# Performance work log

Hardware: AMD Instinct MI355X
Metric: run time of the kernel (lower is better)

## Reference

```python
import jax, jax.numpy as jnp
import numpy as np

B, T, D = 32, 512, 64   # batch, timesteps, latent dim
H, S = 64, 4096         # hidden_size, state_dim
EPS = 1e-6              # flax LayerNorm default epsilon


def _glorot(k, shape):
    lim = np.sqrt(6.0 / (shape[0] + shape[1])).astype(np.float32)
    return jax.random.uniform(k, shape, jnp.float32, -lim, lim)


def setup_inputs() -> dict:
    key = jax.random.key(0)
    ks = jax.random.split(key, 7)
    # gate order in the fused 4H axis: i, f, g, o ; flax inits f-gate bias to 1
    bh = jnp.concatenate([jnp.zeros((H,)), jnp.ones((H,)), jnp.zeros((2 * H,))]).astype(jnp.float32)
    return {
        "enc_outputs": jax.random.normal(ks[0], (B, T, D), jnp.float32),
        "Wx": _glorot(ks[1], (D, 4 * H)),   # input->gates, no bias (flax dense_i)
        "Wh": _glorot(ks[2], (H, 4 * H)),   # hidden->gates
        "bh": bh,
        "W1": _glorot(ks[3], (H, 2 * H)), "b1": jnp.zeros((2 * H,), jnp.float32),
        "g1": jnp.ones((2 * H,), jnp.float32), "be1": jnp.zeros((2 * H,), jnp.float32),
        "W2": _glorot(ks[4], (2 * H, 2 * H)), "b2": jnp.zeros((2 * H,), jnp.float32),
        "g2": jnp.ones((2 * H,), jnp.float32), "be2": jnp.zeros((2 * H,), jnp.float32),
        "Wo": _glorot(ks[5], (2 * H, S)), "bo": jnp.zeros((S,), jnp.float32),
    }


def _layernorm(x, g, b):
    m = x.mean(-1, keepdims=True)
    v = ((x - m) ** 2).mean(-1, keepdims=True)
    return (x - m) * jax.lax.rsqrt(v + EPS) * g + b


def _lstm(enc, Wx, Wh, bh):
    # precompute all input projections in one big GEMM: [B,T,4H]
    xg = jnp.einsum('btd,dg->btg', enc, Wx)

    def step(carry, x_t):
        c, h = carry
        z = x_t + h @ Wh + bh              # [B,4H]
        i, f, g, o = jnp.split(z, 4, axis=-1)
        c = jax.nn.sigmoid(f) * c + jax.nn.sigmoid(i) * jnp.tanh(g)
        h = jax.nn.sigmoid(o) * jnp.tanh(c)
        return (c, h), h

    b = enc.shape[0]
    init = (jnp.zeros((b, H), enc.dtype), jnp.zeros((b, H), enc.dtype))
    _, hs = jax.lax.scan(step, init, xg.swapaxes(0, 1))  # hs: [T,B,H]
    return hs.swapaxes(0, 1)                              # [B,T,H]


def reference(enc_outputs, Wx, Wh, bh, W1, b1, g1, be1, W2, b2, g2, be2, Wo, bo):
    b, t, _ = enc_outputs.shape
    dec = _lstm(enc_outputs, Wx, Wh, bh)            # [B,T,H]
    flat = dec.reshape(b * t, H)
    h = jax.nn.gelu(_layernorm(flat @ W1 + b1, g1, be1))   # flax gelu: tanh approx
    # dropout deterministic (train=False) -> identity
    h = jax.nn.gelu(_layernorm(h @ W2 + b2, g2, be2))
    out = h @ Wo + bo                                # [B*T,S]
    return out.reshape(b, t, S)
```

## Files before the change

kernel.cpp:

```cpp
#include <hip/hip_runtime.h>
#include <hip/hip_bf16.h>

#define T_ 512

typedef __attribute__((ext_vector_type(8))) short short8;
typedef __attribute__((ext_vector_type(4))) float f32x4;

__device__ __forceinline__ float fast_rcp(float x){ return __builtin_amdgcn_rcpf(x); }
__device__ __forceinline__ float sigmoid_f(float x){
  return fast_rcp(1.f + __expf(-x));
}
__device__ __forceinline__ float tanh_f(float x){
  return fmaf(2.f, fast_rcp(1.f + __expf(-2.f*x)), -1.f);
}
__device__ __forceinline__ float gelu_f(float x){
  float u = 0.7978845608028654f*(x + 0.044715f*x*x*x);
  return 0.5f*x*(1.f + tanh_f(u));
}
__device__ __forceinline__ unsigned short bf16_bits(float x){
  __hip_bfloat16 b = __float2bfloat16(x);
  return __builtin_bit_cast(unsigned short, b);
}
__device__ __forceinline__ float bits_f32(unsigned short u){
  return __uint_as_float(((unsigned)u) << 16);
}
__device__ __forceinline__ void bar_lds(){
  asm volatile("s_waitcnt lgkmcnt(0)\n\ts_barrier" ::: "memory");
}

__global__ __launch_bounds__(256) void k_encT(const float* __restrict__ enc,
                                              unsigned short* __restrict__ encB)
{
  int i = blockIdx.x*256 + threadIdx.x;
  int b = i >> 15, t = (i >> 6) & 511, d = i & 63;
  float v = enc[i];
  unsigned short hi = bf16_bits(v);
  float rem = v - bits_f32(hi);
  unsigned short lo = bf16_bits(rem);
  size_t o = (size_t)t*4096 + b*128 + d;
  encB[o]      = hi;
  encB[o + 64] = lo;
}

__global__ __launch_bounds__(256) void k_whxT(const float* __restrict__ Wh,
                                              const float* __restrict__ Wx,
                                              unsigned short* __restrict__ WhxT)
{
  int i = blockIdx.x*256 + threadIdx.x;
  int j = i >> 7, k = i & 127;
  float v = (k < 64) ? Wh[k*256 + j] : Wx[(k - 64)*256 + j];
  WhxT[i] = bf16_bits(v);
}

__global__ __launch_bounds__(256, 1) void k_lstm(const unsigned short* __restrict__ encB,
                                                 const unsigned short* __restrict__ WhxT,
                                                 const float* __restrict__ bh,
                                                 unsigned short* __restrict__ hsb)
{
  __shared__ __align__(16) unsigned short Hb[2][16][72];
  int tid = threadIdx.x;
  int w = tid >> 6, l = tid & 63;
  int m = l & 15, q = l >> 4;
  int bo = blockIdx.x * 16;
  int col0 = 16*w + 4*q;

  const short* Wr = (const short*)WhxT;
  short8 ah[4][2], ax[4][2];
#pragma unroll
  for (int g = 0; g < 4; ++g)
#pragma unroll
    for (int kk = 0; kk < 2; ++kk){
      ah[g][kk] = *(const short8*)(Wr + (64*g + 16*w + m)*128 +      kk*32 + q*8);
      ax[g][kk] = *(const short8*)(Wr + (64*g + 16*w + m)*128 + 64 + kk*32 + q*8);
    }
  f32x4 bb[4];
#pragma unroll
  for (int g = 0; g < 4; ++g){
    bb[g][0] = bh[64*g + 16*w + 4*q + 0];
    bb[g][1] = bh[64*g + 16*w + 4*q + 1];
    bb[g][2] = bh[64*g + 16*w + 4*q + 2];
    bb[g][3] = bh[64*g + 16*w + 4*q + 3];
  }

  for (int i = tid; i < 576; i += 256) ((unsigned int*)&Hb[0][0][0])[i] = 0;

  const unsigned short* encp = encB;
  int em = (bo + m)*128;
  unsigned short* hsrow = hsb + ((size_t)(bo + m)*512)*64 + col0;

  short8 EA0,EA1,EA2,EA3, EB0,EB1,EB2,EB3, EC0,EC1,EC2,EC3, ED0,ED1,ED2,ED3;
  short8 e0,e1,e2,e3;
  e0 = *(const short8*)(encp + 0*4096 + em      + q*8);
  e1 = *(const short8*)(encp + 0*4096 + em + 32 + q*8);
  e2 = *(const short8*)(encp + 0*4096 + em + 64 + q*8);
  e3 = *(const short8*)(encp + 0*4096 + em + 96 + q*8);
  EB0 = *(const short8*)(encp + 1*4096 + em      + q*8);
  EB1 = *(const short8*)(encp + 1*4096 + em + 32 + q*8);
  EB2 = *(const short8*)(encp + 1*4096 + em + 64 + q*8);
  EB3 = *(const short8*)(encp + 1*4096 + em + 96 + q*8);
  EC0 = *(const short8*)(encp + 2*4096 + em      + q*8);
  EC1 = *(const short8*)(encp + 2*4096 + em + 32 + q*8);
  EC2 = *(const short8*)(encp + 2*4096 + em + 64 + q*8);
  EC3 = *(const short8*)(encp + 2*4096 + em + 96 + q*8);
  ED0 = *(const short8*)(encp + 3*4096 + em      + q*8);
  ED1 = *(const short8*)(encp + 3*4096 + em + 32 + q*8);
  ED2 = *(const short8*)(encp + 3*4096 + em + 64 + q*8);
  ED3 = *(const short8*)(encp + 3*4096 + em + 96 + q*8);

  f32x4 xacc[4];
#pragma unroll
  for (int g = 0; g < 4; ++g){
    f32x4 a = __builtin_amdgcn_mfma_f32_16x16x32_bf16(ax[g][0], e0, bb[g], 0,0,0);
    a = __builtin_amdgcn_mfma_f32_16x16x32_bf16(ax[g][1], e1, a, 0,0,0);
    a = __builtin_amdgcn_mfma_f32_16x16x32_bf16(ax[g][0], e2, a, 0,0,0);
    xacc[g] = __builtin_amdgcn_mfma_f32_16x16x32_bf16(ax[g][1], e3, a, 0,0,0);
  }
  float c0 = 0.f, c1 = 0.f, c2 = 0.f, c3 = 0.f;
  __syncthreads();

#define STEP(tt, EU0,EU1,EU2,EU3, EL0,EL1,EL2,EL3)                             \
  {                                                                            \
    const unsigned short* hb = &Hb[(tt) & 1][0][0];                            \
    short8 hv0 = *(const short8*)(hb + m*72 +      q*8);                       \
    short8 hv1 = *(const short8*)(hb + m*72 + 32 + q*8);                       \
    if ((tt) + 4 < T_){                                                        \
      const unsigned short* ep = encp + (size_t)((tt)+4)*4096 + em;            \
      EL0 = *(const short8*)(ep +      q*8);                                   \
      EL1 = *(const short8*)(ep + 32 + q*8);                                   \
      EL2 = *(const short8*)(ep + 64 + q*8);                                   \
      EL3 = *(const short8*)(ep + 96 + q*8);                                   \
    }                                                                          \
    f32x4 z0 = __builtin_amdgcn_mfma_f32_16x16x32_bf16(ah[0][0], hv0, xacc[0], 0,0,0); \
    f32x4 z1 = __builtin_amdgcn_mfma_f32_16x16x32_bf16(ah[1][0], hv0, xacc[1], 0,0,0); \
    f32x4 z2 = __builtin_amdgcn_mfma_f32_16x16x32_bf16(ah[2][0], hv0, xacc[2], 0,0,0); \
    f32x4 z3 = __builtin_amdgcn_mfma_f32_16x16x32_bf16(ah[3][0], hv0, xacc[3], 0,0,0); \
    z0 = __builtin_amdgcn_mfma_f32_16x16x32_bf16(ah[0][1], hv1, z0, 0,0,0);    \
    z1 = __builtin_amdgcn_mfma_f32_16x16x32_bf16(ah[1][1], hv1, z1, 0,0,0);    \
    z2 = __builtin_amdgcn_mfma_f32_16x16x32_bf16(ah[2][1], hv1, z2, 0,0,0);    \
    z3 = __builtin_amdgcn_mfma_f32_16x16x32_bf16(ah[3][1], hv1, z3, 0,0,0);    \
    float h0, h1, h2, h3;                                                      \
    { float si=sigmoid_f(z0[0]), sf=sigmoid_f(z1[0]);                          \
      float tg=tanh_f(z2[0]),    so=sigmoid_f(z3[0]);                          \
      c0 = sf*c0 + si*tg; h0 = so*tanh_f(c0); }                                \
    { float si=sigmoid_f(z0[1]), sf=sigmoid_f(z1[1]);                          \
      float tg=tanh_f(z2[1]),    so=sigmoid_f(z3[1]);                          \
      c1 = sf*c1 + si*tg; h1 = so*tanh_f(c1); }                                \
    { float si=sigmoid_f(z0[2]), sf=sigmoid_f(z1[2]);                          \
      float tg=tanh_f(z2[2]),    so=sigmoid_f(z3[2]);                          \
      c2 = sf*c2 + si*tg; h2 = so*tanh_f(c2); }                                \
    { float si=sigmoid_f(z0[3]), sf=sigmoid_f(z1[3]);                          \
      float tg=tanh_f(z2[3]),    so=sigmoid_f(z3[3]);                          \
      c3 = sf*c3 + si*tg; h3 = so*tanh_f(c3); }                                \
    ushort4 hp;                                                                \
    hp.x = bf16_bits(h0); hp.y = bf16_bits(h1);                                \
    hp.z = bf16_bits(h2); hp.w = bf16_bits(h3);                                \
    *(ushort4*)(&Hb[((tt)+1) & 1][m][col0]) = hp;                              \
    *(ushort4*)(hsrow + (size_t)(tt)*64) = hp;                                 \
    xacc[0] = __builtin_amdgcn_mfma_f32_16x16x32_bf16(ax[0][0], EU0, bb[0], 0,0,0); \
    xacc[1] = __builtin_amdgcn_mfma_f32_16x16x32_bf16(ax[1][0], EU0, bb[1], 0,0,0); \
    xacc[2] = __builtin_amdgcn_mfma_f32_16x16x32_bf16(ax[2][0], EU0, bb[2], 0,0,0); \
    xacc[3] = __builtin_amdgcn_mfma_f32_16x16x32_bf16(ax[3][0], EU0, bb[3], 0,0,0); \
    xacc[0] = __builtin_amdgcn_mfma_f32_16x16x32_bf16(ax[0][1], EU1, xacc[0], 0,0,0); \
    xacc[1] = __builtin_amdgcn_mfma_f32_16x16x32_bf16(ax[1][1], EU1, xacc[1], 0,0,0); \
    xacc[2] = __builtin_amdgcn_mfma_f32_16x16x32_bf16(ax[2][1], EU1, xacc[2], 0,0,0); \
    xacc[3] = __builtin_amdgcn_mfma_f32_16x16x32_bf16(ax[3][1], EU1, xacc[3], 0,0,0); \
    xacc[0] = __builtin_amdgcn_mfma_f32_16x16x32_bf16(ax[0][0], EU2, xacc[0], 0,0,0); \
    xacc[1] = __builtin_amdgcn_mfma_f32_16x16x32_bf16(ax[1][0], EU2, xacc[1], 0,0,0); \
    xacc[2] = __builtin_amdgcn_mfma_f32_16x16x32_bf16(ax[2][0], EU2, xacc[2], 0,0,0); \
    xacc[3] = __builtin_amdgcn_mfma_f32_16x16x32_bf16(ax[3][0], EU2, xacc[3], 0,0,0); \
    xacc[0] = __builtin_amdgcn_mfma_f32_16x16x32_bf16(ax[0][1], EU3, xacc[0], 0,0,0); \
    xacc[1] = __builtin_amdgcn_mfma_f32_16x16x32_bf16(ax[1][1], EU3, xacc[1], 0,0,0); \
    xacc[2] = __builtin_amdgcn_mfma_f32_16x16x32_bf16(ax[2][1], EU3, xacc[2], 0,0,0); \
    xacc[3] = __builtin_amdgcn_mfma_f32_16x16x32_bf16(ax[3][1], EU3, xacc[3], 0,0,0); \
    bar_lds();                          \
  }

  for (int t = 0; t < T_; t += 4){
    STEP(t,   EB0,EB1,EB2,EB3, EA0,EA1,EA2,EA3);
    STEP(t+1, EC0,EC1,EC2,EC3, EB0,EB1,EB2,EB3);
    STEP(t+2, ED0,ED1,ED2,ED3, EC0,EC1,EC2,EC3);
    STEP(t+3, EA0,EA1,EA2,EA3, ED0,ED1,ED2,ED3);
  }
#undef STEP
}

__global__ __launch_bounds__(256) void k_mlp(const unsigned short* __restrict__ hsb,
    const float* __restrict__ W1, const float* __restrict__ b1,
    const float* __restrict__ g1, const float* __restrict__ be1,
    const float* __restrict__ W2, const float* __restrict__ b2,
    const float* __restrict__ g2, const float* __restrict__ be2,
    __hip_bfloat16* __restrict__ h2g)
{
  __shared__ __align__(16) float xs[2][64];
  __shared__ __align__(16) float vs[2][128];
  __shared__ float red[2][2][2];
  int tid = threadIdx.x;
  int jj = tid & 127, rg = tid >> 7;
  int lane = tid & 63;
  int whalf = (tid >> 6) & 1;
  float w1c[64], w2c[128];
#pragma unroll
  for (int k = 0; k < 64; ++k) w1c[k] = W1[k*128 + jj];
#pragma unroll
  for (int k = 0; k < 128; ++k) w2c[k] = W2[k*128 + jj];
  float b1j = b1[jj], g1j = g1[jj], be1j = be1[jj];
  float b2j = b2[jj], g2j = g2[jj], be2j = be2[jj];
  int base = blockIdx.x * 64;
  for (int p = 0; p < 32; ++p){
    int r = base + p*2 + rg;
    if (whalf == 0) xs[rg][lane] = bits_f32(hsb[(size_t)r*64 + lane]);
    __syncthreads();
    float a0 = b1j, a1 = 0.f;
    const float4* x4 = (const float4*)xs[rg];
#pragma unroll
    for (int k4 = 0; k4 < 16; ++k4){
      float4 v = x4[k4];
      a0 = fmaf(v.x, w1c[4*k4+0], a0);
      a1 = fmaf(v.y, w1c[4*k4+1], a1);
      a0 = fmaf(v.z, w1c[4*k4+2], a0);
      a1 = fmaf(v.w, w1c[4*k4+3], a1);
    }
    float a = a0 + a1;
    float s1 = a, s2 = a*a;
#pragma unroll
    for (int off = 32; off > 0; off >>= 1){
      s1 += __shfl_xor(s1, off, 64);
      s2 += __shfl_xor(s2, off, 64);
    }
    if (lane == 0){ red[rg][whalf][0] = s1; red[rg][whalf][1] = s2; }
    __syncthreads();
    s1 = red[rg][0][0] + red[rg][1][0];
    s2 = red[rg][0][1] + red[rg][1][1];
    float mean = s1*(1.f/128.f);
    float var  = s2*(1.f/128.f) - mean*mean;
    float rstd = rsqrtf(var + 1e-6f);
    float y = gelu_f((a - mean)*rstd*g1j + be1j);
    vs[rg][jj] = y;
    __syncthreads();
    float c0 = b2j, c1 = 0.f;
    const float4* v4 = (const float4*)vs[rg];
#pragma unroll
    for (int k4 = 0; k4 < 32; ++k4){
      float4 v = v4[k4];
      c0 = fmaf(v.x, w2c[4*k4+0], c0);
      c1 = fmaf(v.y, w2c[4*k4+1], c1);
      c0 = fmaf(v.z, w2c[4*k4+2], c0);
      c1 = fmaf(v.w, w2c[4*k4+3], c1);
    }
    float cc = c0 + c1;
    float t1 = cc, t2 = cc*cc;
#pragma unroll
    for (int off = 32; off > 0; off >>= 1){
      t1 += __shfl_xor(t1, off, 64);
      t2 += __shfl_xor(t2, off, 64);
    }
    if (lane == 0){ red[rg][whalf][0] = t1; red[rg][whalf][1] = t2; }
    __syncthreads();
    t1 = red[rg][0][0] + red[rg][1][0];
    t2 = red[rg][0][1] + red[rg][1][1];
    mean = t1*(1.f/128.f);
    var  = t2*(1.f/128.f) - mean*mean;
    rstd = rsqrtf(var + 1e-6f);
    float z = gelu_f((cc - mean)*rstd*g2j + be2j);
    h2g[(size_t)r*128 + jj] = __float2bfloat16(z);
  }
}

__global__ __launch_bounds__(256) void k_wot(const float* __restrict__ Wo,
                                             __hip_bfloat16* __restrict__ WoT)
{
  __shared__ __hip_bfloat16 tl[64][130];
  int tid = threadIdx.x;
  int n0 = blockIdx.x * 64;
  for (int idx = tid; idx < 64*128; idx += 256){
    int k = idx >> 6, nl = idx & 63;
    tl[nl][k] = __float2bfloat16(Wo[(size_t)k*4096 + n0 + nl]);
  }
  __syncthreads();
  for (int idx = tid; idx < 64*128; idx += 256){
    int nl = idx >> 7, k = idx & 127;
    WoT[(size_t)(n0 + nl)*128 + k] = tl[nl][k];
  }
}

__global__ __launch_bounds__(256) void k_out(const __hip_bfloat16* __restrict__ h2g,
                                             const __hip_bfloat16* __restrict__ WoT,
                                             const float* __restrict__ bo,
                                             float* __restrict__ out)
{
  int bid0 = blockIdx.x;
  int bid = (bid0 & 7)*512 + (bid0 >> 3);
  int Mb = bid >> 5, Nb = bid & 31;
  int tid = threadIdx.x;
  int w = tid >> 6, l = tid & 63;
  int wm = w >> 1, wn = w & 1;
  int m0 = Mb*128 + wm*64, n0 = Nb*128 + wn*64;
  int lr = l & 15, lk = (l >> 4)*8;
  f32x4 acc[4][4] = {};
  const short* A  = (const short*)WoT;
  const short* Bp = (const short*)h2g;
#pragma unroll
  for (int kk = 0; kk < 4; ++kk){
    int ko = kk*32 + lk;
    short8 av[4], bv[4];
#pragma unroll
    for (int i = 0; i < 4; ++i) av[i] = *(const short8*)(A  + (size_t)(n0 + i*16 + lr)*128 + ko);
#pragma unroll
    for (int i = 0; i < 4; ++i) bv[i] = *(const short8*)(Bp + (size_t)(m0 + i*16 + lr)*128 + ko);
#pragma unroll
    for (int fm = 0; fm < 4; ++fm)
#pragma unroll
      for (int fn = 0; fn < 4; ++fn)
        acc[fm][fn] = __builtin_amdgcn_mfma_f32_16x16x32_bf16(av[fn], bv[fm], acc[fm][fn], 0, 0, 0);
  }
  int nb_ = (l >> 4)*4;
#pragma unroll
  for (int fn = 0; fn < 4; ++fn){
    f32x4 bia = *(const f32x4*)(bo + n0 + fn*16 + nb_);
#pragma unroll
    for (int fm = 0; fm < 4; ++fm){
      size_t row = (size_t)(m0 + fm*16 + lr)*4096;
      __builtin_nontemporal_store(acc[fm][fn] + bia, (f32x4*)(out + row + n0 + fn*16 + nb_));
    }
  }
}

extern "C" void kernel_launch(void* const* d_in, const int* in_sizes, int n_in,
                              void* d_out, int out_size, void* d_ws, size_t ws_size,
                              hipStream_t stream)
{
  const float* enc = (const float*)d_in[0];
  const float* Wx  = (const float*)d_in[1];
  const float* Wh  = (const float*)d_in[2];
  const float* bh  = (const float*)d_in[3];
  const float* W1  = (const float*)d_in[4];
  const float* b1  = (const float*)d_in[5];
  const float* g1  = (const float*)d_in[6];
  const float* be1 = (const float*)d_in[7];
  const float* W2  = (const float*)d_in[8];
  const float* b2  = (const float*)d_in[9];
  const float* g2  = (const float*)d_in[10];
  const float* be2 = (const float*)d_in[11];
  const float* Wo  = (const float*)d_in[12];
  const float* bo  = (const float*)d_in[13];
  float* out = (float*)d_out;

  const size_t encB_bytes = (size_t)512*32*128*2;
  const size_t whx_bytes  = (size_t)256*128*2;
  const size_t hs_bytes   = (size_t)16384*64*2;
  const size_t h2_bytes   = (size_t)16384*128*2;
  const size_t wt_bytes   = (size_t)4096*128*2;
  char* ws = (char*)d_ws;
  unsigned short *encB, *WhxT, *hsb; __hip_bfloat16 *h2g, *WoT;
  if (ws_size >= encB_bytes + whx_bytes + hs_bytes + h2_bytes + wt_bytes){
    encB = (unsigned short*)ws;
    WhxT = (unsigned short*)(ws + encB_bytes);
    hsb  = (unsigned short*)(ws + encB_bytes + whx_bytes);
    h2g  = (__hip_bfloat16*)(ws + encB_bytes + whx_bytes + hs_bytes);
    WoT  = (__hip_bfloat16*)(ws + encB_bytes + whx_bytes + hs_bytes + h2_bytes);
  } else {
    encB = (unsigned short*)d_out;
    WhxT = (unsigned short*)((char*)d_out + encB_bytes);
    hsb  = (unsigned short*)((char*)d_out + encB_bytes + whx_bytes);
    h2g  = (__hip_bfloat16*)ws;
    WoT  = (__hip_bfloat16*)(ws + h2_bytes);
  }

  k_encT<<<4096, 256, 0, stream>>>(enc, encB);
  k_whxT<<<128,  256, 0, stream>>>(Wh, Wx, WhxT);
  k_wot <<<64,   256, 0, stream>>>(Wo, WoT);
  k_lstm<<<2,    256, 0, stream>>>(encB, WhxT, bh, hsb);
  k_mlp <<<256,  256, 0, stream>>>(hsb, W1, b1, g1, be1, W2, b2, g2, be2, h2g);
  k_out <<<4096, 256, 0, stream>>>(h2g, WoT, bo, out);
}
```

Measured before the change: 501.1 us.

## Split LSTM batch across four blocks with duplicated rows and lane shuffles

The LSTM recurrence now runs on 4 blocks of 8 batch rows each instead of 2 blocks of 16. Each batch row is duplicated into the upper half of the 16-row MFMA tile, and lanes exchange gate values with shuffles, so each lane computes only two cell updates per step instead of four. The intent is to shorten the serial per-step latency of the gate nonlinearities. The cost is half-wasted MFMA work and extra shuffles and selects. The enc prefetch bounds check is dropped, and the enc workspace is padded by four timesteps to absorb the reads past the end.

```diff
diff --git a/kernel.cpp b/kernel.cpp
--- a/kernel.cpp
+++ b/kernel.cpp
@@ -61,7 +61,9 @@
   int tid = threadIdx.x;
   int w = tid >> 6, l = tid & 63;
   int m = l & 15, q = l >> 4;
-  int bo = blockIdx.x * 16;
+  int mb = m & 7;
+  bool hi = (m >= 8);
+  int bo = blockIdx.x * 8;
   int col0 = 16*w + 4*q;
 
   const short* Wr = (const short*)WhxT;
@@ -82,11 +84,11 @@
     bb[g][3] = bh[64*g + 16*w + 4*q + 3];
   }
 
-  for (int i = tid; i < 576; i += 256) ((unsigned int*)&Hb[0][0][0])[i] = 0;
+  for (int i = tid; i < 1152; i += 256) ((unsigned int*)&Hb[0][0][0])[i] = 0;
 
   const unsigned short* encp = encB;
-  int em = (bo + m)*128;
-  unsigned short* hsrow = hsb + ((size_t)(bo + m)*512)*64 + col0;
+  int em = (bo + mb)*128;
+  unsigned short* hsrow = hsb + ((size_t)(bo + mb)*512)*64 + col0 + (hi ? 2 : 0);
 
   short8 EA0,EA1,EA2,EA3, EB0,EB1,EB2,EB3, EC0,EC1,EC2,EC3, ED0,ED1,ED2,ED3;
   short8 e0,e1,e2,e3;
@@ -115,7 +117,7 @@
     a = __builtin_amdgcn_mfma_f32_16x16x32_bf16(ax[g][0], e2, a, 0,0,0);
     xacc[g] = __builtin_amdgcn_mfma_f32_16x16x32_bf16(ax[g][1], e3, a, 0,0,0);
   }
-  float c0 = 0.f, c1 = 0.f, c2 = 0.f, c3 = 0.f;
+  float c0 = 0.f, c1 = 0.f;
   __syncthreads();
 
 #define STEP(tt, EU0,EU1,EU2,EU3, EL0,EL1,EL2,EL3)                             \
@@ -123,7 +125,7 @@
     const unsigned short* hb = &Hb[(tt) & 1][0][0];                            \
     short8 hv0 = *(const short8*)(hb + m*72 +      q*8);                       \
     short8 hv1 = *(const short8*)(hb + m*72 + 32 + q*8);                       \
-    if ((tt) + 4 < T_){                                                        \
+    {                     \
       const unsigned short* ep = encp + (size_t)((tt)+4)*4096 + em;            \
       EL0 = *(const short8*)(ep +      q*8);                                   \
       EL1 = *(const short8*)(ep + 32 + q*8);                                   \
@@ -138,24 +140,26 @@
     z1 = __builtin_amdgcn_mfma_f32_16x16x32_bf16(ah[1][1], hv1, z1, 0,0,0);    \
     z2 = __builtin_amdgcn_mfma_f32_16x16x32_bf16(ah[2][1], hv1, z2, 0,0,0);    \
     z3 = __builtin_amdgcn_mfma_f32_16x16x32_bf16(ah[3][1], hv1, z3, 0,0,0);    \
-    float h0, h1, h2, h3;                                                      \
-    { float si=sigmoid_f(z0[0]), sf=sigmoid_f(z1[0]);                          \
-      float tg=tanh_f(z2[0]),    so=sigmoid_f(z3[0]);                          \
+       \
+    float i2 = __shfl_xor(z0[2], 8), i3 = __shfl_xor(z0[3], 8);                \
+    float f2 = __shfl_xor(z1[2], 8), f3 = __shfl_xor(z1[3], 8);                \
+    float g2 = __shfl_xor(z2[2], 8), g3 = __shfl_xor(z2[3], 8);                \
+    float o2 = __shfl_xor(z3[2], 8), o3 = __shfl_xor(z3[3], 8);                \
+    float zia = hi ? i2 : z0[0], zib = hi ? i3 : z0[1];                        \
+    float zfa = hi ? f2 : z1[0], zfb = hi ? f3 : z1[1];                        \
+    float zga = hi ? g2 : z2[0], zgb = hi ? g3 : z2[1];                        \
+    float zoa = hi ? o2 : z3[0], zob = hi ? o3 : z3[1];                        \
+    float h0, h1;                                                              \
+    { float si=sigmoid_f(zia), sf=sigmoid_f(zfa);                              \
+      float tg=tanh_f(zga),    so=sigmoid_f(zoa);                              \
       c0 = sf*c0 + si*tg; h0 = so*tanh_f(c0); }                                \
-    { float si=sigmoid_f(z0[1]), sf=sigmoid_f(z1[1]);                          \
-      float tg=tanh_f(z2[1]),    so=sigmoid_f(z3[1]);                          \
+    { float si=sigmoid_f(zib), sf=sigmoid_f(zfb);                              \
+      float tg=tanh_f(zgb),    so=sigmoid_f(zob);                              \
       c1 = sf*c1 + si*tg; h1 = so*tanh_f(c1); }                                \
-    { float si=sigmoid_f(z0[2]), sf=sigmoid_f(z1[2]);                          \
-      float tg=tanh_f(z2[2]),    so=sigmoid_f(z3[2]);                          \
-      c2 = sf*c2 + si*tg; h2 = so*tanh_f(c2); }                                \
-    { float si=sigmoid_f(z0[3]), sf=sigmoid_f(z1[3]);                          \
-      float tg=tanh_f(z2[3]),    so=sigmoid_f(z3[3]);                          \
-      c3 = sf*c3 + si*tg; h3 = so*tanh_f(c3); }                                \
-    ushort4 hp;                                                                \
+    ushort2 hp;                                                                \
     hp.x = bf16_bits(h0); hp.y = bf16_bits(h1);                                \
-    hp.z = bf16_bits(h2); hp.w = bf16_bits(h3);                                \
-    *(ushort4*)(&Hb[((tt)+1) & 1][m][col0]) = hp;                              \
-    *(ushort4*)(hsrow + (size_t)(tt)*64) = hp;                                 \
+    *(ushort2*)(&Hb[((tt)+1) & 1][mb][col0 + (hi ? 2 : 0)]) = hp;              \
+    *(ushort2*)(hsrow + (size_t)(tt)*64) = hp;                                 \
     xacc[0] = __builtin_amdgcn_mfma_f32_16x16x32_bf16(ax[0][0], EU0, bb[0], 0,0,0); \
     xacc[1] = __builtin_amdgcn_mfma_f32_16x16x32_bf16(ax[1][0], EU0, bb[1], 0,0,0); \
     xacc[2] = __builtin_amdgcn_mfma_f32_16x16x32_bf16(ax[2][0], EU0, bb[2], 0,0,0); \
@@ -172,7 +176,7 @@
     xacc[1] = __builtin_amdgcn_mfma_f32_16x16x32_bf16(ax[1][1], EU3, xacc[1], 0,0,0); \
     xacc[2] = __builtin_amdgcn_mfma_f32_16x16x32_bf16(ax[2][1], EU3, xacc[2], 0,0,0); \
     xacc[3] = __builtin_amdgcn_mfma_f32_16x16x32_bf16(ax[3][1], EU3, xacc[3], 0,0,0); \
-    bar_lds();                          \
+    bar_lds();                                                                 \
   }
 
   for (int t = 0; t < T_; t += 4){
@@ -345,7 +349,7 @@
   const float* bo  = (const float*)d_in[13];
   float* out = (float*)d_out;
 
-  const size_t encB_bytes = (size_t)512*32*128*2;
+  const size_t encB_bytes = (size_t)(512+4)*4096*2;
   const size_t whx_bytes  = (size_t)256*128*2;
   const size_t hs_bytes   = (size_t)16384*64*2;
   const size_t h2_bytes   = (size_t)16384*128*2;
@@ -369,7 +373,7 @@
   k_encT<<<4096, 256, 0, stream>>>(enc, encB);
   k_whxT<<<128,  256, 0, stream>>>(Wh, Wx, WhxT);
   k_wot <<<64,   256, 0, stream>>>(Wo, WoT);
-  k_lstm<<<2,    256, 0, stream>>>(encB, WhxT, bh, hsb);
+  k_lstm<<<4,    256, 0, stream>>>(encB, WhxT, bh, hsb);
   k_mlp <<<256,  256, 0, stream>>>(hsb, W1, b1, g1, be1, W2, b2, g2, be2, h2g);
   k_out <<<4096, 256, 0, stream>>>(h2g, WoT, bo, out);
 }
```

Measured after the change: 465.2 us. 1.08x faster.
